# Optimization experiments

Measured on AMD Instinct MI355X. Metric: run time of the kernel, lower is better.

The kernel has to match this reference:

```python
import jax, jax.numpy as jnp
import numpy as np

N = 50000       # nodes
E = 600000      # edges
ND = 128        # node_dim
ED = 64         # edge_dim
HD = 128        # hidden_dim
EPS = 1e-5

def setup_inputs() -> dict:
    key = jax.random.key(0)
    ks = jax.random.split(key, 32)
    s = 0.05
    rn = lambda k, shp, sc=s: (jax.random.normal(k, shp, dtype=jnp.float32) * sc)
    return {
        "x": jax.random.normal(ks[0], (N, ND), dtype=jnp.float32),
        "edge_index": jax.random.randint(ks[1], (2, E), 0, N),
        "edge_attr": jax.random.normal(ks[2], (E, ED), dtype=jnp.float32),
        # edge_proj: Linear(ED, ND)
        "ep_w": rn(ks[3], (ED, ND)), "ep_b": jnp.zeros((ND,), jnp.float32),
        # gnn1: GATv2Conv(in=2*ND, out=HD, heads=2, edge_dim=ED, concat=False)
        "g1_wl": rn(ks[4], (2 * ND, 2 * HD)), "g1_wr": rn(ks[5], (2 * ND, 2 * HD)),
        "g1_we": rn(ks[6], (ED, 2 * HD)), "g1_att": rn(ks[7], (2, HD)),
        "g1_b": jnp.zeros((HD,), jnp.float32),
        "n1_g": jnp.ones((HD,), jnp.float32), "n1_b": jnp.zeros((HD,), jnp.float32),
        # gnn2: GATv2Conv(in=HD, out=HD, heads=1, edge_dim=ED, concat=False)
        "g2_wl": rn(ks[8], (HD, HD)), "g2_wr": rn(ks[9], (HD, HD)),
        "g2_we": rn(ks[10], (ED, HD)), "g2_att": rn(ks[11], (1, HD)),
        "g2_b": jnp.zeros((HD,), jnp.float32),
        "n2_g": jnp.ones((HD,), jnp.float32), "n2_b": jnp.zeros((HD,), jnp.float32),
        # classifier: Linear(2*HD+ED, HD) -> ReLU -> Linear(HD, HD//2) -> ReLU -> Linear(HD//2, 1)
        "c1_w": rn(ks[12], (2 * HD + ED, HD)), "c1_b": jnp.zeros((HD,), jnp.float32),
        "c2_w": rn(ks[13], (HD, HD // 2)), "c2_b": jnp.zeros((HD // 2,), jnp.float32),
        "c3_w": rn(ks[14], (HD // 2, 1)), "c3_b": jnp.zeros((1,), jnp.float32),
    }

def _scatter_mean(src, index, dim_size):
    tot = jax.ops.segment_sum(src, index, num_segments=dim_size)
    cnt = jax.ops.segment_sum(jnp.ones((src.shape[0],), src.dtype), index, num_segments=dim_size)
    return tot / jnp.maximum(cnt, 1.0)[:, None]

def _segment_softmax(logits, seg, n):
    m = jax.ops.segment_max(logits, seg, num_segments=n)
    m = jnp.where(jnp.isfinite(m), m, 0.0)
    e = jnp.exp(logits - m[seg])
    denom = jax.ops.segment_sum(e, seg, num_segments=n)
    return e / (denom[seg] + 1e-16)

def _gatv2(xf, src, dst, eattr, wl, wr, we, att, b, n, heads, out_c):
    # PyG GATv2: message = leaky_relu(lin_l(x_j) + lin_r(x_i) + lin_edge(e)); alpha = softmax_dst(att . m)
    xl = (xf @ wl).reshape(n, heads, out_c)
    xr = (xf @ wr).reshape(n, heads, out_c)
    ee = (eattr @ we).reshape(-1, heads, out_c)
    msg = jax.nn.leaky_relu(xl[src] + xr[dst] + ee, 0.2)     # [Ea, H, C]
    logits = jnp.einsum('ehc,hc->eh', msg, att)               # [Ea, H]
    alpha = _segment_softmax(logits, dst, n)
    out = jax.ops.segment_sum(xl[src] * alpha[:, :, None], dst, num_segments=n)
    return out.mean(axis=1) + b                               # concat=False -> head mean

def _layernorm(h, g, b):
    mu = h.mean(-1, keepdims=True)
    var = ((h - mu) ** 2).mean(-1, keepdims=True)
    return (h - mu) * jax.lax.rsqrt(var + EPS) * g + b

def reference(x, edge_index, edge_attr, ep_w, ep_b,
              g1_wl, g1_wr, g1_we, g1_att, g1_b, n1_g, n1_b,
              g2_wl, g2_wr, g2_we, g2_att, g2_b, n2_g, n2_b,
              c1_w, c1_b, c2_w, c2_b, c3_w, c3_b):
    n = x.shape[0]
    src, dst = edge_index[0], edge_index[1]
    # node features from edge aggregation
    ee = jax.nn.relu(edge_attr @ ep_w + ep_b)
    x_out = _scatter_mean(ee, src, n)
    x_in = _scatter_mean(ee, dst, n)
    x_input = jnp.concatenate([x_out, x_in], axis=1)          # [N, 2*ND]
    # PyG GATv2Conv default add_self_loops=True, fill_value='mean' over incoming edge_attr
    loop_attr = _scatter_mean(edge_attr, dst, n)
    idx = jnp.arange(n)
    src_a = jnp.concatenate([src, idx])
    dst_a = jnp.concatenate([dst, idx])
    ea_a = jnp.concatenate([edge_attr, loop_attr], axis=0)
    h1 = _gatv2(x_input, src_a, dst_a, ea_a, g1_wl, g1_wr, g1_we, g1_att, g1_b, n, 2, HD)
    h1 = jax.nn.elu(_layernorm(h1, n1_g, n1_b))               # dropout off (eval)
    h2 = _gatv2(h1, src_a, dst_a, ea_a, g2_wl, g2_wr, g2_we, g2_att, g2_b, n, 1, HD)
    h2 = jax.nn.elu(_layernorm(h2, n2_g, n2_b))
    edge_rep = jnp.concatenate([h2[src], h2[dst], edge_attr], axis=1)
    z = jax.nn.relu(edge_rep @ c1_w + c1_b)
    z = jax.nn.relu(z @ c2_w + c2_b)
    return z @ c3_w + c3_b                                    # [E, 1]
```

## Files before the change

### kernel.cpp

```cpp
#include <hip/hip_runtime.h>

constexpr int   NN  = 50000;
constexpr int   NE  = 600000;
constexpr int   EA  = NE + NN;
constexpr int   ND  = 128;
constexpr int   ED  = 64;
constexpr int   HD  = 128;

__global__ void k_hist(const int* __restrict__ src, const int* __restrict__ dst,
                       int* __restrict__ cntS, int* __restrict__ cntD)
{
    int e = blockIdx.x * 256 + threadIdx.x;
    if (e >= NE) return;
    atomicAdd(&cntS[src[e]], 1);
    atomicAdd(&cntD[dst[e]], 1);
}

__global__ __launch_bounds__(1024) void k_scan(
    const int* __restrict__ cntS, const int* __restrict__ cntD,
    int* __restrict__ rpS, int* __restrict__ rpD,
    int* __restrict__ curS, int* __restrict__ curD)
{
    __shared__ int part[1024];
    const int tid = threadIdx.x;
    constexpr int CH = (NN + 1023) / 1024;
    for (int pass = 0; pass < 2; ++pass) {
        const int* cnt = pass ? cntD : cntS;
        int* rp  = pass ? rpD  : rpS;
        int* cur = pass ? curD : curS;
        int i0 = tid * CH, i1 = (i0 + CH < NN) ? i0 + CH : NN;
        int ls = 0;
        for (int i = i0; i < i1; ++i) ls += cnt[i];
        part[tid] = ls;
        __syncthreads();
        for (int off = 1; off < 1024; off <<= 1) {
            int v = (tid >= off) ? part[tid - off] : 0;
            __syncthreads();
            part[tid] += v;
            __syncthreads();
        }
        int run = tid ? part[tid - 1] : 0;
        for (int i = i0; i < i1; ++i) { rp[i] = run; cur[i] = run; run += cnt[i]; }
        if (tid == 1023) rp[NN] = run;
        __syncthreads();
    }
}

__global__ void k_scatter(const int* __restrict__ src, const int* __restrict__ dst,
                          int* __restrict__ curS, int* __restrict__ curD,
                          int* __restrict__ eidS, int* __restrict__ eidD,
                          int* __restrict__ srcS, int* __restrict__ dstS)
{
    int e = blockIdx.x * 256 + threadIdx.x;
    if (e >= NE) return;
    int s = src[e], d = dst[e];
    eidS[atomicAdd(&curS[s], 1)] = e;
    int pd = atomicAdd(&curD[d], 1);
    eidD[pd] = e;
    srcS[pd] = s;
    dstS[pd] = d;
}

__global__ __launch_bounds__(256) void k_node_inputs(
    const float* __restrict__ eattr,
    const int* __restrict__ rpS, const int* __restrict__ eidS,
    const int* __restrict__ rpD, const int* __restrict__ eidD,
    const float* __restrict__ ep_w, const float* __restrict__ ep_b,
    float* __restrict__ x_input, float* __restrict__ loopa)
{
    const int lane = threadIdx.x & 63;
    const int n = blockIdx.x * 4 + (threadIdx.x >> 6);
    if (n >= NN) return;

    float w0r[64], w1r[64];
    #pragma unroll
    for (int k = 0; k < 64; ++k) {
        w0r[k] = ep_w[k * ND + lane];
        w1r[k] = ep_w[k * ND + 64 + lane];
    }
    const float bb0 = ep_b[lane], bb1 = ep_b[64 + lane];

    float aO0 = 0.f, aO1 = 0.f;
    const int s0 = rpS[n], s1 = rpS[n + 1];
    for (int i = s0; i < s1; ++i) {
        const int e = __builtin_amdgcn_readfirstlane(eidS[i]);
        const float* ea = eattr + (long)e * ED;
        float d0 = bb0, d1 = bb1;
        #pragma unroll
        for (int k = 0; k < 64; ++k) {
            float a = ea[k];
            d0 = fmaf(a, w0r[k], d0);
            d1 = fmaf(a, w1r[k], d1);
        }
        aO0 += fmaxf(d0, 0.f);
        aO1 += fmaxf(d1, 0.f);
    }

    float aI0 = 0.f, aI1 = 0.f, la = 0.f;
    const int d0i = rpD[n], d1i = rpD[n + 1];
    for (int i = d0i; i < d1i; ++i) {
        const int e = __builtin_amdgcn_readfirstlane(eidD[i]);
        const float* ea = eattr + (long)e * ED;
        la += ea[lane];
        float d0 = bb0, d1 = bb1;
        #pragma unroll
        for (int k = 0; k < 64; ++k) {
            float a = ea[k];
            d0 = fmaf(a, w0r[k], d0);
            d1 = fmaf(a, w1r[k], d1);
        }
        aI0 += fmaxf(d0, 0.f);
        aI1 += fmaxf(d1, 0.f);
    }

    const float invS = 1.f / (float)((s1 - s0) > 1 ? (s1 - s0) : 1);
    const float invD = 1.f / (float)((d1i - d0i) > 1 ? (d1i - d0i) : 1);
    float* xrow = x_input + (long)n * 256;
    xrow[lane]        = aO0 * invS;
    xrow[64 + lane]   = aO1 * invS;
    xrow[128 + lane]  = aI0 * invD;
    xrow[192 + lane]  = aI1 * invD;
    loopa[(long)n * ED + lane] = la * invD;
}

template<int KD, int NC>
__global__ __launch_bounds__(256) void k_gemm(const float* __restrict__ A,
                                              const float* __restrict__ W,
                                              float* __restrict__ C, int M)
{
    constexpr int CPW = NC / 4;
    __shared__ float a_lds[64][65];
    const int lane = threadIdx.x & 63;
    const int wid  = __builtin_amdgcn_readfirstlane(threadIdx.x >> 6);
    const int r0   = blockIdx.x * 64;
    const int row  = r0 + lane;

    float acc[CPW];
    #pragma unroll
    for (int j = 0; j < CPW; ++j) acc[j] = 0.f;

    for (int k0 = 0; k0 < KD; k0 += 64) {
        __syncthreads();
        for (int r = wid; r < 64; r += 4) {
            int rr = r0 + r;
            a_lds[r][lane] = (rr < M) ? A[(long)rr * KD + k0 + lane] : 0.f;
        }
        __syncthreads();
        for (int k = 0; k < 64; ++k) {
            float a = a_lds[lane][k];
            const float* wrow = W + (long)(k0 + k) * NC + wid * CPW;
            #pragma unroll
            for (int j = 0; j < CPW; ++j) acc[j] = fmaf(a, wrow[j], acc[j]);
        }
    }
    if (row < M) {
        float* crow = C + (long)row * NC + wid * CPW;
        #pragma unroll
        for (int j = 0; j < CPW; ++j) crow[j] = acc[j];
    }
}

template<int HEADS>
__global__ __launch_bounds__(256) void k_gat_logits(
    const float* __restrict__ eattr,
    const int* __restrict__ eidD, const int* __restrict__ srcS, const int* __restrict__ dstS,
    const float* __restrict__ loopa,
    const float* __restrict__ xl, const float* __restrict__ xr,
    const float* __restrict__ we, const float* __restrict__ att,
    float* __restrict__ logits)
{
    constexpr int OC  = HEADS * 128;
    constexpr int CPW = OC / 4;
    __shared__ float ea_lds[64][65];
    __shared__ float p_lds[4][64];
    const int lane = threadIdx.x & 63;
    const int wid  = __builtin_amdgcn_readfirstlane(threadIdx.x >> 6);
    const int p0   = blockIdx.x * 64;

    for (int r = wid; r < 64; r += 4) {
        int pp = p0 + r;
        float v = 0.f;
        if (pp < EA) {
            const float* ap = (pp < NE) ? (eattr + (long)eidD[pp] * ED)
                                        : (loopa + (long)(pp - NE) * ED);
            v = ap[lane];
        }
        ea_lds[r][lane] = v;
    }
    __syncthreads();

    const int p   = p0 + lane;
    const bool val = (p < EA);
    int s = 0, d = 0;
    if (val) {
        if (p < NE) { s = srcS[p]; d = dstS[p]; }
        else        { s = d = p - NE; }
    }
    const int c0 = wid * CPW;

    float acc[CPW];
    #pragma unroll
    for (int j = 0; j < CPW; ++j) acc[j] = 0.f;
    for (int k = 0; k < 64; ++k) {
        float a = ea_lds[lane][k];
        const float* wrow = we + (long)k * OC + c0;
        #pragma unroll
        for (int j = 0; j < CPW; ++j) acc[j] = fmaf(a, wrow[j], acc[j]);
    }

    const float4* xl4 = (const float4*)(xl + (long)s * OC + c0);
    const float4* xr4 = (const float4*)(xr + (long)d * OC + c0);
    float part = 0.f;
    #pragma unroll
    for (int j4 = 0; j4 < CPW / 4; ++j4) {
        float4 a4 = xl4[j4];
        float4 b4 = xr4[j4];
        float m;
        m = acc[4*j4+0] + a4.x + b4.x; m = (m > 0.f) ? m : 0.2f * m; part = fmaf(m, att[c0+4*j4+0], part);
        m = acc[4*j4+1] + a4.y + b4.y; m = (m > 0.f) ? m : 0.2f * m; part = fmaf(m, att[c0+4*j4+1], part);
        m = acc[4*j4+2] + a4.z + b4.z; m = (m > 0.f) ? m : 0.2f * m; part = fmaf(m, att[c0+4*j4+2], part);
        m = acc[4*j4+3] + a4.w + b4.w; m = (m > 0.f) ? m : 0.2f * m; part = fmaf(m, att[c0+4*j4+3], part);
    }
    p_lds[wid][lane] = part;
    __syncthreads();

    if (wid == 0 && val) {
        if (HEADS == 2) {
            logits[(long)p * 2 + 0] = p_lds[0][lane] + p_lds[1][lane];
            logits[(long)p * 2 + 1] = p_lds[2][lane] + p_lds[3][lane];
        } else {
            logits[p] = p_lds[0][lane] + p_lds[1][lane] + p_lds[2][lane] + p_lds[3][lane];
        }
    }
}

template<int HEADS>
__global__ __launch_bounds__(256) void k_gat_reduce(
    const int* __restrict__ rpD, const int* __restrict__ srcS,
    const float* __restrict__ xl, const float* __restrict__ logits,
    const float* __restrict__ bias, const float* __restrict__ g, const float* __restrict__ b,
    float* __restrict__ hout)
{
    constexpr int OC = HEADS * 128;
    const int lane = threadIdx.x & 63;
    const int n = blockIdx.x * 4 + (threadIdx.x >> 6);
    if (n >= NN) return;

    const int base = rpD[n];
    const int deg  = rpD[n + 1] - base;

    float m0 = -1e30f, m1 = -1e30f;
    for (int i = lane; i <= deg; i += 64) {
        long pp = (i < deg) ? (long)(base + i) : (long)(NE + n);
        m0 = fmaxf(m0, logits[pp * HEADS + 0]);
        if (HEADS == 2) m1 = fmaxf(m1, logits[pp * HEADS + 1]);
    }
    #pragma unroll
    for (int off = 32; off; off >>= 1) {
        m0 = fmaxf(m0, __shfl_xor(m0, off));
        if (HEADS == 2) m1 = fmaxf(m1, __shfl_xor(m1, off));
    }

    float s0 = 0.f, s1 = 0.f;
    for (int i = lane; i <= deg; i += 64) {
        long pp = (i < deg) ? (long)(base + i) : (long)(NE + n);
        s0 += __expf(logits[pp * HEADS + 0] - m0);
        if (HEADS == 2) s1 += __expf(logits[pp * HEADS + 1] - m1);
    }
    #pragma unroll
    for (int off = 32; off; off >>= 1) {
        s0 += __shfl_xor(s0, off);
        if (HEADS == 2) s1 += __shfl_xor(s1, off);
    }
    const float inv0 = 1.f / (s0 + 1e-16f);
    const float inv1 = 1.f / (s1 + 1e-16f);

    float a0 = 0.f, a1 = 0.f, a2 = 0.f, a3 = 0.f;
    for (int i = 0; i <= deg; ++i) {
        const bool selfE = (i == deg);
        const long pp = selfE ? (long)(NE + n) : (long)(base + i);
        const int  sN = __builtin_amdgcn_readfirstlane(selfE ? n : srcS[base + i]);
        const float w0 = __expf(logits[pp * HEADS + 0] - m0) * inv0;
        const float* xrow = xl + (long)sN * OC;
        a0 = fmaf(xrow[lane],      w0, a0);
        a1 = fmaf(xrow[64 + lane], w0, a1);
        if (HEADS == 2) {
            const float w1 = __expf(logits[pp * HEADS + 1] - m1) * inv1;
            a2 = fmaf(xrow[128 + lane], w1, a2);
            a3 = fmaf(xrow[192 + lane], w1, a3);
        }
    }

    float v0, v1;
    if (HEADS == 2) { v0 = 0.5f * (a0 + a2); v1 = 0.5f * (a1 + a3); }
    else            { v0 = a0;               v1 = a1; }
    v0 += bias[lane];
    v1 += bias[64 + lane];

    float sum = v0 + v1;
    #pragma unroll
    for (int off = 32; off; off >>= 1) sum += __shfl_xor(sum, off);
    const float mu = sum * (1.f / 128.f);
    const float q0 = v0 - mu, q1 = v1 - mu;
    float vs = q0 * q0 + q1 * q1;
    #pragma unroll
    for (int off = 32; off; off >>= 1) vs += __shfl_xor(vs, off);
    const float rstd = rsqrtf(vs * (1.f / 128.f) + 1e-5f);

    float y0 = q0 * rstd * g[lane]      + b[lane];
    float y1 = q1 * rstd * g[64 + lane] + b[64 + lane];
    hout[(long)n * 128 + lane]      = (y0 > 0.f) ? y0 : (__expf(y0) - 1.f);
    hout[(long)n * 128 + 64 + lane] = (y1 > 0.f) ? y1 : (__expf(y1) - 1.f);
}

__global__ __launch_bounds__(256) void k_classifier(
    const float* __restrict__ Ps, const float* __restrict__ Pd,
    const int* __restrict__ eidD, const int* __restrict__ srcS, const int* __restrict__ dstS,
    const float* __restrict__ eattr,
    const float* __restrict__ c1we, const float* __restrict__ c1b,
    const float* __restrict__ c2w, const float* __restrict__ c2b,
    const float* __restrict__ c3w, const float* __restrict__ c3b,
    float* __restrict__ out)
{
    __shared__ float smem[128 * 65];
    __shared__ float p_lds[4][64];
    const int lane = threadIdx.x & 63;
    const int wid  = __builtin_amdgcn_readfirstlane(threadIdx.x >> 6);
    const int p0   = blockIdx.x * 64;
    const int p    = p0 + lane;
    const bool val = (p < NE);
    const int c0   = wid * 32;

    for (int rr = wid; rr < 64; rr += 4) {
        int pp = p0 + rr;
        smem[rr * 65 + lane] = (pp < NE) ? eattr[(long)eidD[pp] * ED + lane] : 0.f;
    }
    __syncthreads();

    float acc[32];
    #pragma unroll
    for (int j = 0; j < 32; ++j) acc[j] = c1b[c0 + j];
    for (int k = 0; k < 64; ++k) {
        float a = smem[lane * 65 + k];
        const float* wrow = c1we + (long)k * 128 + c0;
        #pragma unroll
        for (int j = 0; j < 32; ++j) acc[j] = fmaf(a, wrow[j], acc[j]);
    }

    const int sN = val ? srcS[p] : 0;
    const int dN = val ? dstS[p] : 0;
    const float4* ps4 = (const float4*)(Ps + (long)sN * 128 + c0);
    const float4* pd4 = (const float4*)(Pd + (long)dN * 128 + c0);
    #pragma unroll
    for (int j4 = 0; j4 < 8; ++j4) {
        float4 a4 = ps4[j4], b4 = pd4[j4];
        acc[4*j4+0] += a4.x + b4.x;
        acc[4*j4+1] += a4.y + b4.y;
        acc[4*j4+2] += a4.z + b4.z;
        acc[4*j4+3] += a4.w + b4.w;
    }

    __syncthreads();
    #pragma unroll
    for (int j = 0; j < 32; ++j) smem[(c0 + j) * 65 + lane] = fmaxf(acc[j], 0.f);
    __syncthreads();

    float acc2[16];
    #pragma unroll
    for (int j = 0; j < 16; ++j) acc2[j] = c2b[wid * 16 + j];
    for (int k = 0; k < 128; ++k) {
        float a = smem[k * 65 + lane];
        const float* wrow = c2w + (long)k * 64 + wid * 16;
        #pragma unroll
        for (int j = 0; j < 16; ++j) acc2[j] = fmaf(a, wrow[j], acc2[j]);
    }
    float part = 0.f;
    #pragma unroll
    for (int j = 0; j < 16; ++j) part = fmaf(fmaxf(acc2[j], 0.f), c3w[wid * 16 + j], part);
    p_lds[wid][lane] = part;
    __syncthreads();
    if (wid == 0 && val)
        out[eidD[p]] = p_lds[0][lane] + p_lds[1][lane] + p_lds[2][lane] + p_lds[3][lane] + c3b[0];
}

extern "C" void kernel_launch(void* const* d_in, const int* in_sizes, int n_in,
                              void* d_out, int out_size, void* d_ws, size_t ws_size,
                              hipStream_t stream)
{
    const int*   edge_index = (const int*)  d_in[1];
    const float* edge_attr  = (const float*)d_in[2];
    const float* ep_w  = (const float*)d_in[3];
    const float* ep_b  = (const float*)d_in[4];
    const float* g1_wl = (const float*)d_in[5];
    const float* g1_wr = (const float*)d_in[6];
    const float* g1_we = (const float*)d_in[7];
    const float* g1_att= (const float*)d_in[8];
    const float* g1_b  = (const float*)d_in[9];
    const float* n1_g  = (const float*)d_in[10];
    const float* n1_b  = (const float*)d_in[11];
    const float* g2_wl = (const float*)d_in[12];
    const float* g2_wr = (const float*)d_in[13];
    const float* g2_we = (const float*)d_in[14];
    const float* g2_att= (const float*)d_in[15];
    const float* g2_b  = (const float*)d_in[16];
    const float* n2_g  = (const float*)d_in[17];
    const float* n2_b  = (const float*)d_in[18];
    const float* c1_w  = (const float*)d_in[19];
    const float* c1_b  = (const float*)d_in[20];
    const float* c2_w  = (const float*)d_in[21];
    const float* c2_b  = (const float*)d_in[22];
    const float* c3_w  = (const float*)d_in[23];
    const float* c3_b  = (const float*)d_in[24];
    const int* src = edge_index;
    const int* dst = edge_index + NE;

    char* wsb = (char*)d_ws;
    size_t o = 0;
    auto alloc = [&](size_t bytes) { void* p = wsb + o; o += (bytes + 255) & ~(size_t)255; return p; };
    int* cntS = (int*)alloc(NN * 4);
    int* cntD = (int*)alloc(NN * 4);
    int* curS = (int*)alloc(NN * 4);
    int* curD = (int*)alloc(NN * 4);
    int* rpS  = (int*)alloc((NN + 1) * 4);
    int* rpD  = (int*)alloc((NN + 1) * 4);
    int* eidS = (int*)alloc((size_t)NE * 4);
    int* eidD = (int*)alloc((size_t)NE * 4);
    int* srcS = (int*)alloc((size_t)NE * 4);
    int* dstS = (int*)alloc((size_t)NE * 4);
    float* loopa   = (float*)alloc((size_t)NN * 64 * 4);
    float* x_input = (float*)alloc((size_t)NN * 256 * 4);
    float* xl1     = (float*)alloc((size_t)NN * 256 * 4);
    float* xr1     = (float*)alloc((size_t)NN * 256 * 4);
    float* logits  = (float*)alloc((size_t)EA * 2 * 4);
    float* h1      = (float*)alloc((size_t)NN * 128 * 4);
    float* xl2 = xl1;
    float* xr2 = xr1;
    float* h2  = x_input;
    float* Ps  = xl1;
    float* Pd  = xr1;

    hipMemsetAsync(d_ws, 0, 2 * ((NN * 4 + 255) & ~255), stream);
    k_hist<<<(NE + 255) / 256, 256, 0, stream>>>(src, dst, cntS, cntD);
    k_scan<<<1, 1024, 0, stream>>>(cntS, cntD, rpS, rpD, curS, curD);
    k_scatter<<<(NE + 255) / 256, 256, 0, stream>>>(src, dst, curS, curD, eidS, eidD, srcS, dstS);

    k_node_inputs<<<(NN + 3) / 4, 256, 0, stream>>>(edge_attr, rpS, eidS, rpD, eidD,
                                                    ep_w, ep_b, x_input, loopa);

    k_gemm<256, 256><<<(NN + 63) / 64, 256, 0, stream>>>(x_input, g1_wl, xl1, NN);
    k_gemm<256, 256><<<(NN + 63) / 64, 256, 0, stream>>>(x_input, g1_wr, xr1, NN);
    k_gat_logits<2><<<(EA + 63) / 64, 256, 0, stream>>>(edge_attr, eidD, srcS, dstS, loopa,
                                                        xl1, xr1, g1_we, g1_att, logits);
    k_gat_reduce<2><<<(NN + 3) / 4, 256, 0, stream>>>(rpD, srcS, xl1, logits, g1_b, n1_g, n1_b, h1);

    k_gemm<128, 128><<<(NN + 63) / 64, 256, 0, stream>>>(h1, g2_wl, xl2, NN);
    k_gemm<128, 128><<<(NN + 63) / 64, 256, 0, stream>>>(h1, g2_wr, xr2, NN);
    k_gat_logits<1><<<(EA + 63) / 64, 256, 0, stream>>>(edge_attr, eidD, srcS, dstS, loopa,
                                                        xl2, xr2, g2_we, g2_att, logits);
    k_gat_reduce<1><<<(NN + 3) / 4, 256, 0, stream>>>(rpD, srcS, xl2, logits, g2_b, n2_g, n2_b, h2);

    k_gemm<128, 128><<<(NN + 63) / 64, 256, 0, stream>>>(h2, c1_w,             Ps, NN);
    k_gemm<128, 128><<<(NN + 63) / 64, 256, 0, stream>>>(h2, c1_w + 128 * 128, Pd, NN);
    k_classifier<<<(NE + 63) / 64, 256, 0, stream>>>(Ps, Pd, eidD, srcS, dstS, edge_attr,
                                                     c1_w + 256 * 128, c1_b, c2_w, c2_b, c3_w, c3_b,
                                                     (float*)d_out);
}
```

Before: 2.257 ms.

## Split node-input work across four waves per node and unroll edge loops by two

k_node_inputs now launches one block per node, with four waves covering the out/in side and the two 64-column halves. Each wave holds 64 weight registers instead of 128, which should raise occupancy and spread the per-node work. Its edge loop and the gat_reduce aggregation loop now process two edges per iteration with independent accumulators, exposing more memory-level parallelism. The cost is redundant edge_attr reads, since each edge row is now read by two waves, and per-node blocks that sit mostly idle on low-degree nodes.

New measurement: 2.285 ms. No clear change (+1.2%).

```diff
diff --git a/kernel.cpp b/kernel.cpp
--- a/kernel.cpp
+++ b/kernel.cpp
@@ -61,7 +61,7 @@
     dstS[pd] = d;
 }
 
-__global__ __launch_bounds__(256) void k_node_inputs(
+__global__ __launch_bounds__(256, 2) void k_node_inputs(
     const float* __restrict__ eattr,
     const int* __restrict__ rpS, const int* __restrict__ eidS,
     const int* __restrict__ rpD, const int* __restrict__ eidD,
@@ -69,58 +69,54 @@
     float* __restrict__ x_input, float* __restrict__ loopa)
 {
     const int lane = threadIdx.x & 63;
-    const int n = blockIdx.x * 4 + (threadIdx.x >> 6);
-    if (n >= NN) return;
-
-    float w0r[64], w1r[64];
-    #pragma unroll
-    for (int k = 0; k < 64; ++k) {
-        w0r[k] = ep_w[k * ND + lane];
-        w1r[k] = ep_w[k * ND + 64 + lane];
-    }
-    const float bb0 = ep_b[lane], bb1 = ep_b[64 + lane];
-
-    float aO0 = 0.f, aO1 = 0.f;
-    const int s0 = rpS[n], s1 = rpS[n + 1];
-    for (int i = s0; i < s1; ++i) {
-        const int e = __builtin_amdgcn_readfirstlane(eidS[i]);
+    const int wid  = threadIdx.x >> 6;
+    const int side = wid >> 1;
+    const int half = wid & 1;
+    const int n    = blockIdx.x;
+    const int c    = half * 64 + lane;
+
+    float w[64];
+    #pragma unroll
+    for (int k = 0; k < 64; ++k) w[k] = ep_w[k * ND + c];
+    const float bb = ep_b[c];
+
+    const int* rp  = side ? rpD  : rpS;
+    const int* eid = side ? eidD : eidS;
+    const int i0 = rp[n], i1 = rp[n + 1];
+    const bool doLoopa = (side == 1) && (half == 0);
+
+    float acc = 0.f, accB = 0.f, la = 0.f;
+    int i = i0;
+    for (; i + 1 < i1; i += 2) {
+        const int eAi = __builtin_amdgcn_readfirstlane(eid[i]);
+        const int eBi = __builtin_amdgcn_readfirstlane(eid[i + 1]);
+        const float* eaA = eattr + (long)eAi * ED;
+        const float* eaB = eattr + (long)eBi * ED;
+        if (doLoopa) la += eaA[lane] + eaB[lane];
+        float dA = bb, dB = bb;
+        #pragma unroll
+        for (int k = 0; k < 64; ++k) {
+            dA = fmaf(eaA[k], w[k], dA);
+            dB = fmaf(eaB[k], w[k], dB);
+        }
+        acc  += fmaxf(dA, 0.f);
+        accB += fmaxf(dB, 0.f);
+    }
+    if (i < i1) {
+        const int e = __builtin_amdgcn_readfirstlane(eid[i]);
         const float* ea = eattr + (long)e * ED;
-        float d0 = bb0, d1 = bb1;
-        #pragma unroll
-        for (int k = 0; k < 64; ++k) {
-            float a = ea[k];
-            d0 = fmaf(a, w0r[k], d0);
-            d1 = fmaf(a, w1r[k], d1);
-        }
-        aO0 += fmaxf(d0, 0.f);
-        aO1 += fmaxf(d1, 0.f);
-    }
-
-    float aI0 = 0.f, aI1 = 0.f, la = 0.f;
-    const int d0i = rpD[n], d1i = rpD[n + 1];
-    for (int i = d0i; i < d1i; ++i) {
-        const int e = __builtin_amdgcn_readfirstlane(eidD[i]);
-        const float* ea = eattr + (long)e * ED;
-        la += ea[lane];
-        float d0 = bb0, d1 = bb1;
-        #pragma unroll
-        for (int k = 0; k < 64; ++k) {
-            float a = ea[k];
-            d0 = fmaf(a, w0r[k], d0);
-            d1 = fmaf(a, w1r[k], d1);
-        }
-        aI0 += fmaxf(d0, 0.f);
-        aI1 += fmaxf(d1, 0.f);
-    }
-
-    const float invS = 1.f / (float)((s1 - s0) > 1 ? (s1 - s0) : 1);
-    const float invD = 1.f / (float)((d1i - d0i) > 1 ? (d1i - d0i) : 1);
-    float* xrow = x_input + (long)n * 256;
-    xrow[lane]        = aO0 * invS;
-    xrow[64 + lane]   = aO1 * invS;
-    xrow[128 + lane]  = aI0 * invD;
-    xrow[192 + lane]  = aI1 * invD;
-    loopa[(long)n * ED + lane] = la * invD;
+        if (doLoopa) la += ea[lane];
+        float d = bb;
+        #pragma unroll
+        for (int k = 0; k < 64; ++k) d = fmaf(ea[k], w[k], d);
+        acc += fmaxf(d, 0.f);
+    }
+    acc += accB;
+
+    const int cnt = i1 - i0;
+    const float inv = 1.f / (float)(cnt > 1 ? cnt : 1);
+    x_input[(long)n * 256 + side * 128 + c] = acc * inv;
+    if (doLoopa) loopa[(long)n * ED + lane] = la * inv;
 }
 
 template<int KD, int NC>
@@ -276,7 +272,30 @@
     const float inv1 = 1.f / (s1 + 1e-16f);
 
     float a0 = 0.f, a1 = 0.f, a2 = 0.f, a3 = 0.f;
-    for (int i = 0; i <= deg; ++i) {
+    float c0 = 0.f, c1 = 0.f, c2 = 0.f, c3 = 0.f;
+    int i = 0;
+    for (; i + 1 < deg; i += 2) {
+        const long pA = base + i, pB = base + i + 1;
+        const int  sA = __builtin_amdgcn_readfirstlane(srcS[pA]);
+        const int  sB = __builtin_amdgcn_readfirstlane(srcS[pB]);
+        const float* xrA = xl + (long)sA * OC;
+        const float* xrB = xl + (long)sB * OC;
+        const float wA0 = __expf(logits[pA * HEADS + 0] - m0) * inv0;
+        const float wB0 = __expf(logits[pB * HEADS + 0] - m0) * inv0;
+        a0 = fmaf(xrA[lane],      wA0, a0);
+        a1 = fmaf(xrA[64 + lane], wA0, a1);
+        c0 = fmaf(xrB[lane],      wB0, c0);
+        c1 = fmaf(xrB[64 + lane], wB0, c1);
+        if (HEADS == 2) {
+            const float wA1 = __expf(logits[pA * HEADS + 1] - m1) * inv1;
+            const float wB1 = __expf(logits[pB * HEADS + 1] - m1) * inv1;
+            a2 = fmaf(xrA[128 + lane], wA1, a2);
+            a3 = fmaf(xrA[192 + lane], wA1, a3);
+            c2 = fmaf(xrB[128 + lane], wB1, c2);
+            c3 = fmaf(xrB[192 + lane], wB1, c3);
+        }
+    }
+    for (; i <= deg; ++i) {
         const bool selfE = (i == deg);
         const long pp = selfE ? (long)(NE + n) : (long)(base + i);
         const int  sN = __builtin_amdgcn_readfirstlane(selfE ? n : srcS[base + i]);
@@ -290,6 +309,7 @@
             a3 = fmaf(xrow[192 + lane], w1, a3);
         }
     }
+    a0 += c0; a1 += c1; a2 += c2; a3 += c3;
 
     float v0, v1;
     if (HEADS == 2) { v0 = 0.5f * (a0 + a2); v1 = 0.5f * (a1 + a3); }
@@ -444,8 +464,8 @@
     k_scan<<<1, 1024, 0, stream>>>(cntS, cntD, rpS, rpD, curS, curD);
     k_scatter<<<(NE + 255) / 256, 256, 0, stream>>>(src, dst, curS, curD, eidS, eidD, srcS, dstS);
 
-    k_node_inputs<<<(NN + 3) / 4, 256, 0, stream>>>(edge_attr, rpS, eidS, rpD, eidD,
-                                                    ep_w, ep_b, x_input, loopa);
+    k_node_inputs<<<NN, 256, 0, stream>>>(edge_attr, rpS, eidS, rpD, eidD,
+                                          ep_w, ep_b, x_input, loopa);
 
     k_gemm<256, 256><<<(NN + 63) / 64, 256, 0, stream>>>(x_input, g1_wl, xl1, NN);
     k_gemm<256, 256><<<(NN + 63) / 64, 256, 0, stream>>>(x_input, g1_wr, xr1, NN);
```
